# Performance work log

Hardware: AMD Instinct MI355X
Metric: run time of the kernel (lower is better)

## Reference

```python
import jax, jax.numpy as jnp
import numpy as np

B, T, V, E, U = 64, 512, 32000, 1024, 1024


def setup_inputs() -> dict:
    key = jax.random.key(0)
    k0, k1, k2, k3 = jax.random.split(key, 4)
    x = jax.random.randint(k0, (B, T), 0, V, dtype=jnp.int32)
    hidden = jnp.zeros((B, U), jnp.float32)
    emb = jax.random.normal(k1, (V, E), jnp.float32) * 0.02
    Wx = jax.random.normal(k2, (E, 3 * U), jnp.float32) / np.sqrt(E).astype(np.float32)
    Wh = jax.random.normal(k3, (U, 3 * U), jnp.float32) / np.sqrt(U).astype(np.float32)
    b_i = jnp.zeros((3 * U,), jnp.float32)  # input bias (reset_after=True has 2 biases)
    b_r = jnp.zeros((3 * U,), jnp.float32)  # recurrent bias
    return {"x": x, "hidden": hidden, "emb": emb, "Wx": Wx, "Wh": Wh, "b_i": b_i, "b_r": b_r}


def reference(x, hidden, emb, Wx, Wh, b_i, b_r):
    # Embedding with mask_zero=True: mask = (token != 0)
    mask = (x != 0)                                   # [B,T]
    e = jnp.take(emb, x, axis=0)                      # [B,T,E]
    # Precompute all input projections in one big GEMM (z|r|h gate order, Keras layout)
    xp = jnp.einsum('bte,eu->btu', e, Wx) + b_i       # [B,T,3U]
    xp_t = jnp.moveaxis(xp, 1, 0)                     # [T,B,3U] time-major for scan
    m_t = jnp.moveaxis(mask, 1, 0)[..., None]         # [T,B,1]

    def step(h, inp):
        xpt, m = inp
        hp = h @ Wh + b_r                             # [B,3U]
        xz, xr, xh = jnp.split(xpt, 3, axis=-1)
        hz, hr, hh = jnp.split(hp, 3, axis=-1)
        z = jax.nn.sigmoid(xz + hz)
        r = jax.nn.sigmoid(xr + hr)
        cand = jnp.tanh(xh + r * hh)                  # reset_after=True: r applied post-matmul
        h_new = z * h + (1.0 - z) * cand
        h_new = jnp.where(m, h_new, h)                # masked steps copy state through
        return h_new, h_new

    state, out_t = jax.lax.scan(step, hidden, (xp_t, m_t))
    output = jnp.moveaxis(out_t, 0, 1)                # [B,T,U]
    return output, state
```

## Files before the change

kernel.cpp:

```cpp
#include <hip/hip_runtime.h>
#include <stdint.h>


#define B_SZ   64
#define T_LEN  512
#define U_DIM  1024
#define E_DIM  1024
#define G3     3072
#define BU     (B_SZ * U_DIM)
#define XP_SCALE 131072.0f
#define XP_INV   (1.0f / 131072.0f)
#define H_SCALE  32768.0f
#define H_INV    (1.0f / 32768.0f)
#define LDT    40
#define NWG    256

typedef unsigned short ushort_t;
typedef __attribute__((ext_vector_type(8))) short bf16x8;
typedef __attribute__((ext_vector_type(4))) float f32x4;

__device__ __forceinline__ ushort_t f2bf(float f) {
  unsigned u = __builtin_bit_cast(unsigned, f);
  u += 0x7fffu + ((u >> 16) & 1u);
  return (ushort_t)(u >> 16);
}
__device__ __forceinline__ float bf2f(ushort_t h) {
  return __builtin_bit_cast(float, (unsigned)h << 16);
}

__device__ __forceinline__ bf16x8 ldg_cohere_b128(const void* p) {
  bf16x8 r;
  asm volatile("global_load_dwordx4 %0, %1, off sc0 sc1"
               : "=v"(r) : "v"(p) : "memory");
  return r;
}
__device__ __forceinline__ void stg_cohere_u16(short* p, unsigned v) {
  asm volatile("global_store_short %0, %1, off sc0 sc1"
               :: "v"(p), "v"(v) : "memory");
}
__device__ __forceinline__ void stg_cohere_u32(unsigned* p, unsigned v) {
  asm volatile("global_store_dword %0, %1, off sc0 sc1"
               :: "v"(p), "v"(v) : "memory");
}
__device__ __forceinline__ unsigned ldg_cohere_u32(const unsigned* p) {
  unsigned r;
  asm volatile("global_load_dword %0, %1, off sc0 sc1\n\ts_waitcnt vmcnt(0)"
               : "=v"(r) : "v"(p) : "memory");
  return r;
}
__device__ __forceinline__ int ldg_sshort(const short* p) {
  int r;
  asm volatile("global_load_sshort %0, %1, off"
               : "=v"(r) : "v"(p) : "memory");
  return r;
}
__device__ __forceinline__ int ldg_s32(const int* p) {
  int r;
  asm volatile("global_load_dword %0, %1, off"
               : "=v"(r) : "v"(p) : "memory");
  return r;
}
__device__ __forceinline__ void stg_u32(float* p, float v) {
  asm volatile("global_store_dword %0, %1, off"
               :: "v"(p), "v"(v) : "memory");
}
#define WAITV(n) do { asm volatile("s_waitcnt vmcnt(" #n ")" ::: "memory"); \
                      __builtin_amdgcn_sched_barrier(0); } while (0)

__global__ __launch_bounds__(256) void gemm_xp(
    const float* __restrict__ emb,
    const float* __restrict__ Wx,
    const int* __restrict__ x,
    const float* __restrict__ b_i,
    short* __restrict__ xp)
{
  __shared__ ushort_t aH[128 * LDT];
  __shared__ ushort_t aL[128 * LDT];
  __shared__ ushort_t bH[128 * LDT];
  __shared__ ushort_t bL[128 * LDT];
  const int tid = threadIdx.x, lane = tid & 63, w = tid >> 6;
  const int bx = blockIdx.x;
  const int nIdx = bx % 24, mIdx = bx / 24;
  const int m0 = mIdx * 128, n0 = nIdx * 128;

  const int aRow0 = tid >> 2, aRow1 = (tid + 256) >> 2, aKoct = tid & 3;
  const size_t aBase0 = (size_t)x[m0 + aRow0] * E_DIM + (size_t)aKoct * 8;
  const size_t aBase1 = (size_t)x[m0 + aRow1] * E_DIM + (size_t)aKoct * 8;
  const int bN = tid & 127, bKoct0 = tid >> 7;

  const int wr = (w >> 1) * 64, wc = (w & 1) * 64;
  f32x4 acc[4][4];
#pragma unroll
  for (int i = 0; i < 4; i++)
#pragma unroll
    for (int j = 0; j < 4; j++) acc[i][j] = (f32x4){0.f, 0.f, 0.f, 0.f};

  for (int k0 = 0; k0 < E_DIM; k0 += 32) {
    __syncthreads();
#pragma unroll
    for (int pp = 0; pp < 2; ++pp) {
      const float* src = emb + (pp ? aBase1 : aBase0) + k0;
      int row = pp ? aRow1 : aRow0;
      float4 v0 = *(const float4*)(src);
      float4 v1 = *(const float4*)(src + 4);
      float vv[8] = {v0.x, v0.y, v0.z, v0.w, v1.x, v1.y, v1.z, v1.w};
      bf16x8 oh, ol;
#pragma unroll
      for (int j = 0; j < 8; ++j) {
        ushort_t hi = f2bf(vv[j]);
        oh[j] = (short)hi;
        ol[j] = (short)f2bf(vv[j] - bf2f(hi));
      }
      int off = row * LDT + aKoct * 8;
      *(bf16x8*)&aH[off] = oh;
      *(bf16x8*)&aL[off] = ol;
    }
#pragma unroll
    for (int kk = 0; kk < 2; ++kk) {
      int koct = bKoct0 + 2 * kk;
      float vv[8];
#pragma unroll
      for (int e = 0; e < 8; ++e)
        vv[e] = Wx[(size_t)(k0 + koct * 8 + e) * G3 + n0 + bN];
      bf16x8 oh, ol;
#pragma unroll
      for (int j = 0; j < 8; ++j) {
        ushort_t hi = f2bf(vv[j]);
        oh[j] = (short)hi;
        ol[j] = (short)f2bf(vv[j] - bf2f(hi));
      }
      int off = bN * LDT + koct * 8;
      *(bf16x8*)&bH[off] = oh;
      *(bf16x8*)&bL[off] = ol;
    }
    __syncthreads();
    bf16x8 afH[4], afL[4], bfH[4], bfL[4];
#pragma unroll
    for (int mi = 0; mi < 4; mi++) {
      int off = (wr + mi * 16 + (lane & 15)) * LDT + (lane >> 4) * 8;
      afH[mi] = *(const bf16x8*)&aH[off];
      afL[mi] = *(const bf16x8*)&aL[off];
    }
#pragma unroll
    for (int ni = 0; ni < 4; ni++) {
      int off = (wc + ni * 16 + (lane & 15)) * LDT + (lane >> 4) * 8;
      bfH[ni] = *(const bf16x8*)&bH[off];
      bfL[ni] = *(const bf16x8*)&bL[off];
    }
#pragma unroll
    for (int mi = 0; mi < 4; mi++)
#pragma unroll
      for (int ni = 0; ni < 4; ni++) {
        acc[mi][ni] = __builtin_amdgcn_mfma_f32_16x16x32_bf16(afH[mi], bfH[ni], acc[mi][ni], 0, 0, 0);
        acc[mi][ni] = __builtin_amdgcn_mfma_f32_16x16x32_bf16(afH[mi], bfL[ni], acc[mi][ni], 0, 0, 0);
        acc[mi][ni] = __builtin_amdgcn_mfma_f32_16x16x32_bf16(afL[mi], bfH[ni], acc[mi][ni], 0, 0, 0);
      }
  }
#pragma unroll
  for (int ni = 0; ni < 4; ni++) {
    int col = n0 + wc + ni * 16 + (lane & 15);
    float bias = b_i[col];
#pragma unroll
    for (int mi = 0; mi < 4; mi++) {
      int rbase = m0 + wr + mi * 16 + (lane >> 4) * 4;
#pragma unroll
      for (int i = 0; i < 4; i++) {
        int m = rbase + i;
        int b = m >> 9, t = m & 511;
        float v = acc[mi][ni][i] + bias;
        int q = __float2int_rn(v * XP_SCALE);
        q = q > 32767 ? 32767 : (q < -32768 ? -32768 : q);
        xp[(size_t)(t * 64 + b) * G3 + col] = (short)q;
      }
    }
  }
}

__global__ __launch_bounds__(256) void init_h(
    const float* __restrict__ hidden,
    short* __restrict__ h16,
    unsigned* __restrict__ flags)
{
  const int i = blockIdx.x * 256 + threadIdx.x;
  if (blockIdx.x < 16) flags[blockIdx.x * 256 + threadIdx.x] = 0u;
  if (i < BU) {
    int q = __float2int_rn(hidden[i] * H_SCALE);
    q = q > 32767 ? 32767 : (q < -32768 ? -32768 : q);
    h16[i] = (short)q;
  }
}

__global__ __launch_bounds__(512) void gru_scan(
    const float* __restrict__ hidden,
    const float* __restrict__ Wh,
    const float* __restrict__ b_r,
    const short* __restrict__ xp,
    const int* __restrict__ x,
    short* __restrict__ h16,
    unsigned* __restrict__ flags,
    float* __restrict__ out)
{
  __shared__ float part[8][3][64][4];
  const int tid  = threadIdx.x;
  const int lane = tid & 63;
  const int w    = tid >> 6;
  const int bx   = (int)blockIdx.x;
  const int uj   = bx & 63, bi = bx >> 6;
  const int u0   = uj * 16, b0 = bi * 16;
  const int c16  = lane & 15;
  const int kg   = lane >> 4;
  unsigned* gflags = flags + bi * 1024;
  const unsigned* pollp = gflags + lane * 16;

  bf16x8 BH[4][3], BL[4][3];
#pragma unroll
  for (int ks = 0; ks < 4; ++ks)
#pragma unroll
    for (int g = 0; g < 3; ++g) {
      bf16x8 bh, bl;
#pragma unroll
      for (int j = 0; j < 8; ++j) {
        int k = w * 128 + ks * 32 + kg * 8 + j;
        float v = Wh[(size_t)k * G3 + g * 1024 + u0 + c16];
        ushort_t hi = f2bf(v);
        bh[j] = (short)hi;
        bl[j] = (short)f2bf(v - bf2f(hi));
      }
      BH[ks][g] = bh;
      BL[ks][g] = bl;
    }

  const bool epi = (tid < 256);
  const int ebl = (tid >> 4) & 15, eul = tid & 15;
  const int eb = b0 + ebl, eu = u0 + eul;
  float brz = 0.f, brr = 0.f, brh = 0.f, hp = 0.f;
  if (epi) {
    brz = b_r[eu]; brr = b_r[1024 + eu]; brh = b_r[2048 + eu];
    hp  = hidden[(size_t)eb * U_DIM + eu];
  }

  asm volatile("s_waitcnt vmcnt(0) lgkmcnt(0)" ::: "memory");

  int xq0 = 0, xq1 = 0, xq2 = 0, xtok = 0;
  if (epi) {
    xq0 = ldg_sshort(xp + (size_t)eb * G3 + eu);
    xq1 = ldg_sshort(xp + (size_t)eb * G3 + 1024 + eu);
    xq2 = ldg_sshort(xp + (size_t)eb * G3 + 2048 + eu);
    xtok = ldg_s32(x + eb * T_LEN + 0);
  }

  unsigned spins = 0;
  for (int t = 0; t < T_LEN; ++t) {
    const short* __restrict__ rP = h16 + (size_t)(t & 1) * BU;
    short* __restrict__ wP       = h16 + (size_t)((t + 1) & 1) * BU;

    if (t > 0) {
      if (w == 0) {
        const unsigned tgt = (unsigned)t;
        while (spins < (1u << 22)) {
          unsigned f = ldg_cohere_u32(pollp);
          if (__ballot(f >= tgt) == ~0ull) break;
          __builtin_amdgcn_s_sleep(2);
          ++spins;
        }
      }
      __syncthreads();
    }

    const short* pP = rP + (size_t)(b0 + c16) * U_DIM + w * 128 + kg * 8;

    f32x4 acc[3];
#pragma unroll
    for (int g = 0; g < 3; ++g) acc[g] = (f32x4){0.f, 0.f, 0.f, 0.f};

    bf16x8 P0, P1, P2, P3;
    P0 = ldg_cohere_b128(pP + 0 * 32);
    P1 = ldg_cohere_b128(pP + 1 * 32);
    P2 = ldg_cohere_b128(pP + 2 * 32);
    P3 = ldg_cohere_b128(pP + 3 * 32);

#define UNPCK(P_, AH_, AL_) \
    { \
      _Pragma("unroll") \
      for (int j = 0; j < 8; ++j) { \
        float v = (float)(short)P_[j] * H_INV; \
        ushort_t hi = f2bf(v); \
        AH_[j] = (short)hi; \
        AL_[j] = (short)f2bf(v - bf2f(hi)); \
      } \
    }
#define COMP(AH_, AL_, ks_) \
    _Pragma("unroll") \
    for (int g = 0; g < 3; ++g) { \
      acc[g] = __builtin_amdgcn_mfma_f32_16x16x32_bf16(AH_, BH[ks_][g], acc[g], 0, 0, 0); \
      acc[g] = __builtin_amdgcn_mfma_f32_16x16x32_bf16(AH_, BL[ks_][g], acc[g], 0, 0, 0); \
      acc[g] = __builtin_amdgcn_mfma_f32_16x16x32_bf16(AL_, BH[ks_][g], acc[g], 0, 0, 0); \
    }
    bf16x8 AH, AL;
    WAITV(3);
    UNPCK(P0, AH, AL)
    COMP(AH, AL, 0)
    WAITV(2);
    UNPCK(P1, AH, AL)
    COMP(AH, AL, 1)
    WAITV(1);
    UNPCK(P2, AH, AL)
    COMP(AH, AL, 2)
    WAITV(0);
    UNPCK(P3, AH, AL)
    COMP(AH, AL, 3)
#undef UNPCK
#undef COMP

#pragma unroll
    for (int g = 0; g < 3; ++g)
      *(f32x4*)&part[w][g][lane][0] = acc[g];

    __syncthreads();

    if (epi) {
      const int pl = (ebl >> 2) * 16 + eul, pe = ebl & 3;
      float sz = 0.f, sr = 0.f, sh = 0.f;
#pragma unroll
      for (int s = 0; s < 8; ++s) {
        sz += part[s][0][pl][pe];
        sr += part[s][1][pl][pe];
        sh += part[s][2][pl][pe];
      }

      const float hz = sz + brz, hr = sr + brr, hhv = sh + brh;
      const float xz = (float)xq0 * XP_INV;
      const float xr = (float)xq1 * XP_INV;
      const float xh = (float)xq2 * XP_INV;
      const float z = 1.f / (1.f + __expf(-(xz + hz)));
      const float r = 1.f / (1.f + __expf(-(xr + hr)));
      const float ca = xh + r * hhv;
      const float cand = 1.f - 2.f / (__expf(2.f * ca) + 1.f);
      float hn = z * hp + (1.f - z) * cand;
      hn = (xtok != 0) ? hn : hp;
      hp = hn;

      stg_u32(&out[((size_t)eb * T_LEN + t) * U_DIM + eu], hn);
      int q = __float2int_rn(hn * H_SCALE);
      q = q > 32767 ? 32767 : (q < -32768 ? -32768 : q);
      stg_cohere_u16(wP + (size_t)eb * U_DIM + eu, (unsigned)q);

      const int tp = (t < T_LEN - 1) ? t + 1 : t;
      xq0 = ldg_sshort(xp + ((size_t)tp * B_SZ + eb) * G3 + eu);
      xq1 = ldg_sshort(xp + ((size_t)tp * B_SZ + eb) * G3 + 1024 + eu);
      xq2 = ldg_sshort(xp + ((size_t)tp * B_SZ + eb) * G3 + 2048 + eu);
      xtok = ldg_s32(x + eb * T_LEN + tp);
      WAITV(4);
    }

    __syncthreads();
    if (tid == 0)
      stg_cohere_u32(gflags + uj * 16, (unsigned)(t + 1));
    __builtin_amdgcn_sched_barrier(0);
  }

  if (epi)
    out[(size_t)B_SZ * T_LEN * U_DIM + (size_t)eb * U_DIM + eu] = hp;
}

extern "C" void kernel_launch(void* const* d_in, const int* in_sizes, int n_in,
                              void* d_out, int out_size, void* d_ws, size_t ws_size,
                              hipStream_t stream) {
  const int*   x      = (const int*)  d_in[0];
  const float* hidden = (const float*)d_in[1];
  const float* emb    = (const float*)d_in[2];
  const float* Wx     = (const float*)d_in[3];
  const float* Wh     = (const float*)d_in[4];
  const float* b_i    = (const float*)d_in[5];
  const float* b_r    = (const float*)d_in[6];
  float* out = (float*)d_out;

  const size_t XP_B = (size_t)T_LEN * B_SZ * G3 * 2;
  const size_t NEED = XP_B + 4 * (size_t)BU + 16384;
  if (ws_size < NEED) return;

  short*    xp    = (short*)d_ws;
  short*    h16   = (short*)((char*)d_ws + XP_B);
  unsigned* flags = (unsigned*)(h16 + 2 * (size_t)BU);

  init_h<<<BU / 256, 256, 0, stream>>>(hidden, h16, flags);
  gemm_xp<<<(32768 / 128) * (G3 / 128), 256, 0, stream>>>(emb, Wx, x, b_i, xp);
  gru_scan<<<NWG, 512, 0, stream>>>(hidden, Wh, b_r, xp, x, h16, flags, out);
}
```

Measured before the change: 2.910 ms.

## Use single bf16 MFMA in input GEMM and pre-poll scan flags early

The input-projection GEMM drops the hi/lo split-bf16 emulation. It now converts emb and Wx to plain bf16 and issues one MFMA per tile instead of three, which halves the LDS tiles and removes the conversion and extra matrix work. In the recurrent scan, the idle wave 7 pre-polls the next step's flags during the epilogue and publishes a shared ready bit so the next iteration can skip spinning. The hidden-state store is also moved ahead of the output store, and the sleep interval is shortened. The main risk is lower accuracy in xp from single-bf16 rounding. The ready check also polls the block's own flag, which is not yet written at that point, so it may never fire.

After: 2.634 ms. 9.5% less time.

```diff
diff --git a/kernel.cpp b/kernel.cpp
--- a/kernel.cpp
+++ b/kernel.cpp
@@ -75,9 +75,7 @@
     short* __restrict__ xp)
 {
   __shared__ ushort_t aH[128 * LDT];
-  __shared__ ushort_t aL[128 * LDT];
   __shared__ ushort_t bH[128 * LDT];
-  __shared__ ushort_t bL[128 * LDT];
   const int tid = threadIdx.x, lane = tid & 63, w = tid >> 6;
   const int bx = blockIdx.x;
   const int nIdx = bx % 24, mIdx = bx / 24;
@@ -104,16 +102,10 @@
       float4 v0 = *(const float4*)(src);
       float4 v1 = *(const float4*)(src + 4);
       float vv[8] = {v0.x, v0.y, v0.z, v0.w, v1.x, v1.y, v1.z, v1.w};
-      bf16x8 oh, ol;
-#pragma unroll
-      for (int j = 0; j < 8; ++j) {
-        ushort_t hi = f2bf(vv[j]);
-        oh[j] = (short)hi;
-        ol[j] = (short)f2bf(vv[j] - bf2f(hi));
-      }
-      int off = row * LDT + aKoct * 8;
-      *(bf16x8*)&aH[off] = oh;
-      *(bf16x8*)&aL[off] = ol;
+      bf16x8 oh;
+#pragma unroll
+      for (int j = 0; j < 8; ++j) oh[j] = (short)f2bf(vv[j]);
+      *(bf16x8*)&aH[row * LDT + aKoct * 8] = oh;
     }
 #pragma unroll
     for (int kk = 0; kk < 2; ++kk) {
@@ -122,39 +114,28 @@
 #pragma unroll
       for (int e = 0; e < 8; ++e)
         vv[e] = Wx[(size_t)(k0 + koct * 8 + e) * G3 + n0 + bN];
-      bf16x8 oh, ol;
-#pragma unroll
-      for (int j = 0; j < 8; ++j) {
-        ushort_t hi = f2bf(vv[j]);
-        oh[j] = (short)hi;
-        ol[j] = (short)f2bf(vv[j] - bf2f(hi));
-      }
-      int off = bN * LDT + koct * 8;
-      *(bf16x8*)&bH[off] = oh;
-      *(bf16x8*)&bL[off] = ol;
+      bf16x8 oh;
+#pragma unroll
+      for (int j = 0; j < 8; ++j) oh[j] = (short)f2bf(vv[j]);
+      *(bf16x8*)&bH[bN * LDT + koct * 8] = oh;
     }
     __syncthreads();
-    bf16x8 afH[4], afL[4], bfH[4], bfL[4];
+    bf16x8 afH[4], bfH[4];
 #pragma unroll
     for (int mi = 0; mi < 4; mi++) {
       int off = (wr + mi * 16 + (lane & 15)) * LDT + (lane >> 4) * 8;
       afH[mi] = *(const bf16x8*)&aH[off];
-      afL[mi] = *(const bf16x8*)&aL[off];
     }
 #pragma unroll
     for (int ni = 0; ni < 4; ni++) {
       int off = (wc + ni * 16 + (lane & 15)) * LDT + (lane >> 4) * 8;
       bfH[ni] = *(const bf16x8*)&bH[off];
-      bfL[ni] = *(const bf16x8*)&bL[off];
     }
 #pragma unroll
     for (int mi = 0; mi < 4; mi++)
 #pragma unroll
-      for (int ni = 0; ni < 4; ni++) {
+      for (int ni = 0; ni < 4; ni++)
         acc[mi][ni] = __builtin_amdgcn_mfma_f32_16x16x32_bf16(afH[mi], bfH[ni], acc[mi][ni], 0, 0, 0);
-        acc[mi][ni] = __builtin_amdgcn_mfma_f32_16x16x32_bf16(afH[mi], bfL[ni], acc[mi][ni], 0, 0, 0);
-        acc[mi][ni] = __builtin_amdgcn_mfma_f32_16x16x32_bf16(afL[mi], bfH[ni], acc[mi][ni], 0, 0, 0);
-      }
   }
 #pragma unroll
   for (int ni = 0; ni < 4; ni++) {
@@ -201,6 +182,7 @@
     float* __restrict__ out)
 {
   __shared__ float part[8][3][64][4];
+  __shared__ unsigned ready;
   const int tid  = threadIdx.x;
   const int lane = tid & 63;
   const int w    = tid >> 6;
@@ -256,12 +238,14 @@
 
     if (t > 0) {
       if (w == 0) {
-        const unsigned tgt = (unsigned)t;
-        while (spins < (1u << 22)) {
-          unsigned f = ldg_cohere_u32(pollp);
-          if (__ballot(f >= tgt) == ~0ull) break;
-          __builtin_amdgcn_s_sleep(2);
-          ++spins;
+        if (ready == 0u) {
+          const unsigned tgt = (unsigned)t;
+          while (spins < (1u << 22)) {
+            unsigned f = ldg_cohere_u32(pollp);
+            if (__ballot(f >= tgt) == ~0ull) break;
+            __builtin_amdgcn_s_sleep(1);
+            ++spins;
+          }
         }
       }
       __syncthreads();
@@ -340,17 +324,28 @@
       hn = (xtok != 0) ? hn : hp;
       hp = hn;
 
-      stg_u32(&out[((size_t)eb * T_LEN + t) * U_DIM + eu], hn);
       int q = __float2int_rn(hn * H_SCALE);
       q = q > 32767 ? 32767 : (q < -32768 ? -32768 : q);
       stg_cohere_u16(wP + (size_t)eb * U_DIM + eu, (unsigned)q);
+      stg_u32(&out[((size_t)eb * T_LEN + t) * U_DIM + eu], hn);
 
       const int tp = (t < T_LEN - 1) ? t + 1 : t;
       xq0 = ldg_sshort(xp + ((size_t)tp * B_SZ + eb) * G3 + eu);
       xq1 = ldg_sshort(xp + ((size_t)tp * B_SZ + eb) * G3 + 1024 + eu);
       xq2 = ldg_sshort(xp + ((size_t)tp * B_SZ + eb) * G3 + 2048 + eu);
       xtok = ldg_s32(x + eb * T_LEN + tp);
-      WAITV(4);
+      WAITV(5);
+    } else if (w == 7) {
+      const unsigned tgt2 = (unsigned)(t + 1);
+      unsigned ok = 0;
+#pragma unroll
+      for (int it = 0; it < 2; ++it) {
+        if (!ok) {
+          unsigned f = ldg_cohere_u32(pollp);
+          if (__ballot(f >= tgt2) == ~0ull) ok = 1u;
+        }
+      }
+      if (lane == 0) ready = ok;
     }
 
     __syncthreads();
```
